# Performance work log

Hardware: AMD Instinct MI355X
Metric: run time of the kernel (lower is better)

The kernel has to match this reference:

```python
import jax, jax.numpy as jnp
import numpy as np

SEQ, B, IN_DIM, HID, DEPTH = 200, 128, 1024, 1024, 5
P_IN, P_HID = 0.75, 0.25  # input_dropout, hidden_dropout


def setup_inputs() -> dict:
    key = jax.random.key(0)
    ks = jax.random.split(key, 12)
    inp = jax.random.normal(ks[0], (SEQ, B, IN_DIM), dtype=jnp.float32)
    hidden = jax.random.normal(ks[1], (B, HID), dtype=jnp.float32) * 0.1

    # make_dropout_mask: bernoulli(keep_p) / keep_p ; tied_noise=True -> shared H/T masks
    keep_in, keep_hid = 1.0 - P_IN, 1.0 - P_HID
    h_mask = jax.random.bernoulli(ks[2], keep_in, (B, IN_DIM)).astype(jnp.float32) / keep_in
    s_mask = jax.random.bernoulli(ks[3], keep_hid, (B, HID)).astype(jnp.float32) / keep_hid

    # nn.Linear default init: U(-1/sqrt(fan_in), 1/sqrt(fan_in)); W stored (out, in)
    si, sh = 1.0 / np.sqrt(IN_DIM), 1.0 / np.sqrt(HID)
    u = lambda k, shape, s: jax.random.uniform(k, shape, jnp.float32, -s, s)
    Wih = u(ks[4], (HID, IN_DIM), si)
    bih = u(ks[5], (HID,), si)
    Wit = u(ks[6], (HID, IN_DIM), si)
    bit = u(ks[7], (HID,), si)
    Wh = u(ks[8], (DEPTH, HID, HID), sh)
    Wt = u(ks[9], (DEPTH, HID, HID), sh)
    # layer 0 recurrent Linears have bias=False -> zero bias row
    bh = u(ks[10], (DEPTH, HID), sh).at[0].set(0.0)
    bt = u(ks[11], (DEPTH, HID), sh).at[0].set(0.0)

    return {"inp": inp, "hidden": hidden, "h_mask": h_mask, "s_mask": s_mask,
            "Wih": Wih, "bih": bih, "Wit": Wit, "bit": bit,
            "Wh": Wh, "bh": bh, "Wt": Wt, "bt": bt}


def reference(inp, hidden, h_mask, s_mask, Wih, bih, Wit, bit, Wh, bh, Wt, bt):
    # tied_noise=True: same input mask for H and T paths, same hidden mask for both gates
    x = inp * h_mask  # (S, B, in) broadcast mask over seq
    H = jnp.einsum('sbi,oi->sbo', x, Wih) + bih  # precomputed input contribution
    T = jnp.einsum('sbi,oi->sbo', x, Wit) + bit

    def step(s, HT):
        H_t, T_t = HT  # (B, HID) each
        for l in range(DEPTH):
            sm = s * s_mask  # hidden dropout mask, shared H/T (tied_noise)
            if l == 0:
                Hl = jnp.tanh(H_t + jnp.einsum('bi,oi->bo', sm, Wh[l]) + bh[l])
                Tl = jax.nn.sigmoid(T_t + jnp.einsum('bi,oi->bo', sm, Wt[l]) + bt[l])
            else:
                Hl = jnp.tanh(jnp.einsum('bi,oi->bo', sm, Wh[l]) + bh[l])
                Tl = jax.nn.sigmoid(jnp.einsum('bi,oi->bo', sm, Wt[l]) + bt[l])
            # coupled highway: s_l = (h - s_{l-1}) * t + s_{l-1}
            s = (Hl - s) * Tl + s
        return s, s

    last, outs = jax.lax.scan(step, hidden, (H, T))
    return outs, last
```

## Files before the change

### kernel.cpp

```cpp
#include <hip/hip_runtime.h>
#include <hip/hip_bf16.h>
#include <stdint.h>

#define SEQ    200
#define BATCH  128
#define NHID   1024
#define NDEPTH 5
#define NBLK   256
#define GRP_BLK 128
#define CPB    8
#define PANEL  ((size_t)BATCH * NHID)
#define SB     (SEQ * BATCH)

typedef __bf16 bf16x8 __attribute__((ext_vector_type(8)));
typedef float  f32x4  __attribute__((ext_vector_type(4)));
typedef uint32_t u32x4 __attribute__((ext_vector_type(4)));
typedef __hip_bfloat16 bf16_t;

__device__ __forceinline__ f32x4 mfma16(bf16x8 a, bf16x8 b, f32x4 c) {
    return __builtin_amdgcn_mfma_f32_16x16x32_bf16(a, b, c, 0, 0, 0);
}
__device__ __forceinline__ bf16x8 as_bf16x8(u32x4 x) {
    union { u32x4 u; bf16x8 b; } t; t.u = x; return t.b;
}
__device__ __forceinline__ unsigned short f32_to_bf16_bits(float f) {
    uint32_t x = __float_as_uint(f);
    uint32_t r = ((x >> 16) & 1u) + 0x7fffu;
    return (unsigned short)((x + r) >> 16);
}
template<int PAT>
__device__ __forceinline__ float swzf(float v) {
    return __int_as_float(__builtin_amdgcn_ds_swizzle(__float_as_int(v), PAT));
}
template<int PAT>
__device__ __forceinline__ uint32_t swzu(uint32_t v) {
    return (uint32_t)__builtin_amdgcn_ds_swizzle((int)v, PAT);
}

__global__ void k_cast_bf16(const float* __restrict__ src, bf16_t* __restrict__ dst, int n) {
    for (int i = blockIdx.x * blockDim.x + threadIdx.x; i < n; i += gridDim.x * blockDim.x)
        dst[i] = __float2bfloat16(src[i]);
}

__global__ void k_init_smb(const float* __restrict__ hidden, const float* __restrict__ s_mask,
                           bf16_t* __restrict__ smb, int n) {
    for (int i = blockIdx.x * blockDim.x + threadIdx.x; i < n; i += gridDim.x * blockDim.x)
        smb[i] = __float2bfloat16(hidden[i] * s_mask[i]);
}

__global__ __launch_bounds__(256) void k_ht(
    const float* __restrict__ inp, const float* __restrict__ h_mask,
    const bf16_t* __restrict__ Wihb, const float* __restrict__ bih,
    const bf16_t* __restrict__ Witb, const float* __restrict__ bitv,
    _Float16* __restrict__ ht)
{
    const int lane = threadIdx.x & 63;
    const int w    = threadIdx.x >> 6;
    const int r0   = blockIdx.y * 32 + (w >> 1) * 16;
    const int c0   = blockIdx.x * 64 + (w & 1) * 32;
    const int lr   = lane & 15;
    const int kg   = lane >> 4;

    f32x4 aH0 = {0,0,0,0}, aH1 = {0,0,0,0}, aT0 = {0,0,0,0}, aT1 = {0,0,0,0};
    const int R = r0 + lr;
    const float* ap = inp + (size_t)R * NHID + kg * 8;
    const float* mp = h_mask + (size_t)(R & 127) * NHID + kg * 8;
    const bf16_t* Bh = Wihb + (size_t)(c0 + lr) * NHID + kg * 8;
    const bf16_t* Bt = Witb + (size_t)(c0 + lr) * NHID + kg * 8;

    for (int k = 0; k < NHID; k += 32) {
        f32x4 x0 = *(const f32x4*)(ap + k), x1 = *(const f32x4*)(ap + k + 4);
        f32x4 m0 = *(const f32x4*)(mp + k), m1 = *(const f32x4*)(mp + k + 4);
        union { bf16_t h[8]; bf16x8 v; } af;
        #pragma unroll
        for (int q = 0; q < 4; ++q) {
            af.h[q]     = __float2bfloat16(x0[q] * m0[q]);
            af.h[q + 4] = __float2bfloat16(x1[q] * m1[q]);
        }
        bf16x8 bh0 = *(const bf16x8*)(Bh + k);
        bf16x8 bh1 = *(const bf16x8*)(Bh + (size_t)16 * NHID + k);
        bf16x8 bt0 = *(const bf16x8*)(Bt + k);
        bf16x8 bt1 = *(const bf16x8*)(Bt + (size_t)16 * NHID + k);
        aH0 = mfma16(af.v, bh0, aH0);
        aH1 = mfma16(af.v, bh1, aH1);
        aT0 = mfma16(af.v, bt0, aT0);
        aT1 = mfma16(af.v, bt1, aT1);
    }

    const int n0 = c0 + lr, n1 = n0 + 16;
    #pragma unroll
    for (int j = 0; j < 4; ++j) {
        const int R2 = r0 + kg * 4 + j;
        const int t = R2 >> 7, b = R2 & 127;
        _Float16* hrow = ht + ((size_t)(t * 2 + 0) * BATCH + b) * NHID;
        _Float16* trow = ht + ((size_t)(t * 2 + 1) * BATCH + b) * NHID;
        hrow[n0] = (_Float16)(aH0[j] + bih[n0]);
        hrow[n1] = (_Float16)(aH1[j] + bih[n1]);
        trow[n0] = (_Float16)(aT0[j] + bitv[n0]);
        trow[n1] = (_Float16)(aT1[j] + bitv[n1]);
    }
}

#define LDU(i, OFF)  asm volatile("global_load_dwordx4 %0, %1, off offset:" OFF " sc0 sc1" \
                                  : "=v"(AR[i]) : "v"(aptr));
#define ISSUE32(M) \
    M(0,"0")    M(1,"64")   M(2,"128")  M(3,"192")  M(4,"256")  M(5,"320")  M(6,"384")  M(7,"448") \
    M(8,"512")  M(9,"576")  M(10,"640") M(11,"704") M(12,"768") M(13,"832") M(14,"896") M(15,"960") \
    M(16,"1024") M(17,"1088") M(18,"1152") M(19,"1216") M(20,"1280") M(21,"1344") M(22,"1408") M(23,"1472") \
    M(24,"1536") M(25,"1600") M(26,"1664") M(27,"1728") M(28,"1792") M(29,"1856") M(30,"1920") M(31,"1984")
#define WAITV(N) do { asm volatile("s_waitcnt vmcnt(" #N ")" ::: "memory"); \
                      __builtin_amdgcn_sched_barrier(0x187); } while (0)
#define CHUNK_LDS(c) do { _Pragma("unroll") \
    for (int e = 0; e < 8; ++e) { \
        const int off = (kg * 16 + ((c) * 8 + e) * 64) ^ xmask; \
        bf16x8 bf = *(const bf16x8*)(rowb + off); \
        acc = mfma16(as_bf16x8(AR[(c) * 8 + e]), bf, acc); } } while (0)

__global__ __launch_bounds__(256, 1) void k_rhn_persist(
    const float* __restrict__ hidden, const float* __restrict__ s_mask,
    const float* __restrict__ Wh,  const float* __restrict__ bh,
    const float* __restrict__ Wt,  const float* __restrict__ bt,
    const _Float16* __restrict__ ht,
    bf16_t* __restrict__ smbA, bf16_t* __restrict__ smbB,
    unsigned int* __restrict__ flags,
    float* __restrict__ out)
{
    extern __shared__ char wlds[];
    const int tid  = threadIdx.x;
    const int lane = tid & 63;
    const int wv   = tid >> 6;
    const int g    = blockIdx.x >> 7;
    const int gb   = blockIdx.x & (GRP_BLK - 1);
    const int c0   = gb * CPB;
    const int lr   = lane & 15;
    const int kg   = lane >> 4;
    const int wbase = g * 64 + wv * 16;
    const int cc   = c0 + (lr & 7);
    const bool isT = lr >= 8;
    const int xmask = (lr & 7) << 4;

    for (int row = wv; row < 80; row += 4) {
        const int l = row >> 4, r = row & 15;
        const float* src = ((r < 8) ? Wh : Wt) + ((size_t)l * NHID + c0 + (r & 7)) * NHID;
        char* rb = wlds + (size_t)row * 2048;
        const int X = (r & 7) << 4;
        #pragma unroll
        for (int u = 0; u < 2; ++u) {
            union { bf16_t h[8]; u32x4 v; } pk;
            #pragma unroll
            for (int q = 0; q < 8; ++q)
                pk.h[q] = __float2bfloat16(src[lane * 16 + u * 8 + q]);
            *(u32x4*)(rb + ((lane * 32 + u * 16) ^ X)) = pk.v;
        }
    }

    float biasl[NDEPTH];
    #pragma unroll
    for (int l = 0; l < NDEPTH; ++l)
        biasl[l] = isT ? bt[(size_t)l * NHID + cc] : bh[(size_t)l * NHID + cc];
    float sreg[4], smk[4];
    #pragma unroll
    for (int j = 0; j < 4; ++j) {
        const int row = wbase + kg * 4 + j;
        sreg[j] = hidden[(size_t)row * NHID + cc];
        smk[j]  = s_mask[(size_t)row * NHID + cc];
    }

    __syncthreads();

    const size_t aoff = (size_t)(wbase + lr) * NHID + kg * 8;
    unsigned int rv = 0;
    int par = 0;

    for (int t = 0; t < SEQ; ++t) {
        #pragma unroll
        for (int l = 0; l < NDEPTH; ++l) {
            const bf16_t* Abuf = par ? smbB : smbA;
            bf16_t*       An   = par ? smbA : smbB;
            f32x4 acc = {0.f, 0.f, 0.f, 0.f};
            u32x4 AR[32];

            {
                const bf16_t* aptr = Abuf + aoff;
                const char* rowb = wlds + (size_t)(l * 16 + lr) * 2048;
                ISSUE32(LDU)
                WAITV(24); CHUNK_LDS(0);
                WAITV(16); CHUNK_LDS(1);
                WAITV(8);  CHUNK_LDS(2);
                WAITV(0);  CHUNK_LDS(3);
            }
            if (l == 0) {
                const _Float16* hp = ht + (size_t)(t * 2 + (isT ? 1 : 0)) * PANEL + cc;
                #pragma unroll
                for (int j = 0; j < 4; ++j)
                    acc[j] += (float)hp[(size_t)(wbase + kg * 4 + j) * NHID];
            }

            const float vb = biasl[l];
            #pragma unroll
            for (int j = 0; j < 4; ++j) {
                float v = acc[j] + vb;
                float o = swzf<0x201F>(v);
                float Hv = tanhf(v);
                float Tv = 1.f / (1.f + __expf(-o));
                float sv = sreg[j];
                float sn = (Hv - sv) * Tv + sv;
                sreg[j] = sn;
                const int row = wbase + kg * 4 + j;

                uint32_t a  = (uint32_t)f32_to_bf16_bits(sn * smk[j]);
                uint32_t b1 = swzu<0x041F>(a);
                uint32_t w  = (a & 0xffffu) | (b1 << 16);
                uint32_t c2 = swzu<0x081F>(w);
                uint32_t e1 = swzu<0x101F>(w);
                uint32_t e2 = swzu<0x101F>(c2);
                if (lr == 0) {
                    uint64_t q0 = (uint64_t)w  | ((uint64_t)c2 << 32);
                    uint64_t q1 = (uint64_t)e1 | ((uint64_t)e2 << 32);
                    uint64_t* p = (uint64_t*)(An + (size_t)row * NHID + c0);
                    __hip_atomic_store(p,     q0, __ATOMIC_RELAXED, __HIP_MEMORY_SCOPE_AGENT);
                    __hip_atomic_store(p + 1, q1, __ATOMIC_RELAXED, __HIP_MEMORY_SCOPE_AGENT);
                }
                if (l == NDEPTH - 1 && lr < 8) {
                    out[((size_t)t * BATCH + row) * NHID + cc] = sn;
                    if (t == SEQ - 1)
                        out[(size_t)SEQ * BATCH * NHID + (size_t)row * NHID + cc] = sn;
                }
            }

            ++rv;
            if (!(t == SEQ - 1 && l == NDEPTH - 1)) {
                __syncthreads();
                if (tid == 0)
                    __hip_atomic_store(&flags[(g * GRP_BLK + gb) * 16], rv,
                                       __ATOMIC_RELAXED, __HIP_MEMORY_SCOPE_AGENT);
                if (tid < 64) {
                    const unsigned int* p0 = &flags[(g * GRP_BLK + lane) * 16];
                    const unsigned int* p1 = &flags[(g * GRP_BLK + 64 + lane) * 16];
                    for (;;) {
                        unsigned int f0 = __hip_atomic_load(p0, __ATOMIC_RELAXED,
                                                            __HIP_MEMORY_SCOPE_AGENT);
                        unsigned int f1 = __hip_atomic_load(p1, __ATOMIC_RELAXED,
                                                            __HIP_MEMORY_SCOPE_AGENT);
                        if (__all(f0 >= rv && f1 >= rv)) break;
                        __builtin_amdgcn_s_sleep(2);
                    }
                }
                __syncthreads();
            }
            par ^= 1;
        }
    }
}

extern "C" void kernel_launch(void* const* d_in, const int* in_sizes, int n_in,
                              void* d_out, int out_size, void* d_ws, size_t ws_size,
                              hipStream_t stream) {
    (void)in_sizes; (void)n_in; (void)out_size; (void)ws_size;

    const float* inp    = (const float*)d_in[0];
    const float* hidden = (const float*)d_in[1];
    const float* h_mask = (const float*)d_in[2];
    const float* s_mask = (const float*)d_in[3];
    const float* Wih    = (const float*)d_in[4];
    const float* bih    = (const float*)d_in[5];
    const float* Wit    = (const float*)d_in[6];
    const float* bitv   = (const float*)d_in[7];
    const float* Wh     = (const float*)d_in[8];
    const float* bh     = (const float*)d_in[9];
    const float* Wt     = (const float*)d_in[10];
    const float* bt     = (const float*)d_in[11];
    float* out = (float*)d_out;

    _Float16* ht   = (_Float16*)d_ws;
    bf16_t* Wihb   = (bf16_t*)(ht + (size_t)SEQ * 2 * PANEL);
    bf16_t* Witb   = Wihb + (size_t)NHID * NHID;
    bf16_t* smbA   = Witb + (size_t)NHID * NHID;
    bf16_t* smbB   = smbA + PANEL;
    unsigned int* flags = (unsigned int*)(smbB + PANEL);

    hipMemsetAsync(flags, 0, NBLK * 16 * sizeof(unsigned int), stream);
    k_cast_bf16<<<dim3(512), dim3(256), 0, stream>>>(Wih, Wihb, NHID * NHID);
    k_cast_bf16<<<dim3(512), dim3(256), 0, stream>>>(Wit, Witb, NHID * NHID);
    k_init_smb<<<dim3(64), dim3(256), 0, stream>>>(hidden, s_mask, smbA, BATCH * NHID);
    k_ht<<<dim3(NHID / 64, SB / 32), dim3(256), 0, stream>>>(
        inp, h_mask, Wihb, bih, Witb, bitv, ht);

    const size_t ldsBytes = (size_t)80 * 2048;
    hipFuncSetAttribute((const void*)k_rhn_persist,
                        hipFuncAttributeMaxDynamicSharedMemorySize, (int)ldsBytes);
    k_rhn_persist<<<dim3(NBLK), dim3(256), ldsBytes, stream>>>(
        hidden, s_mask, Wh, bh, Wt, bt, ht, smbA, smbB, flags, out);
}
```

Baseline: 7.644 ms.

## Relay hidden-state panel into per-XCD mirror buffers with two-level barrier

Each layer step now copies the freshly written bf16 hidden panel from the global buffer into a per-XCD mirror, split across the blocks on that XCD. The GEMM A-loads then read the mirror with sc0 only, so they can hit the XCD-local L2 instead of bypassing it. The grid-wide barrier now waits on all 256 blocks rather than two groups of 128, and an extra per-XCD barrier follows the relay. This trades cross-die uncached reads for an extra copy pass and a second synchronization every layer step. The mirrors reuse the Wih/Wit bf16 workspace, which is free after k_ht finishes.

```diff
diff --git a/kernel.cpp b/kernel.cpp
--- a/kernel.cpp
+++ b/kernel.cpp
@@ -10,6 +10,7 @@
 #define GRP_BLK 128
 #define CPB    8
 #define PANEL  ((size_t)BATCH * NHID)
+#define PANELB ((size_t)BATCH * NHID * 2)
 #define SB     (SEQ * BATCH)
 
 typedef __bf16 bf16x8 __attribute__((ext_vector_type(8)));
@@ -35,6 +36,11 @@
 template<int PAT>
 __device__ __forceinline__ uint32_t swzu(uint32_t v) {
     return (uint32_t)__builtin_amdgcn_ds_swizzle((int)v, PAT);
+}
+__device__ __forceinline__ int get_xcc_id() {
+    int x;
+    asm volatile("s_getreg_b32 %0, hwreg(HW_REG_XCC_ID)" : "=s"(x));
+    return x & 7;
 }
 
 __global__ void k_cast_bf16(const float* __restrict__ src, bf16_t* __restrict__ dst, int n) {
@@ -101,8 +107,8 @@
     }
 }
 
-#define LDU(i, OFF)  asm volatile("global_load_dwordx4 %0, %1, off offset:" OFF " sc0 sc1" \
-                                  : "=v"(AR[i]) : "v"(aptr));
+#define LDU(i, OFF) asm volatile("global_load_dwordx4 %0, %1, off offset:" OFF " sc0" \
+                                 : "=v"(AR[i]) : "v"(aptr));
 #define ISSUE32(M) \
     M(0,"0")    M(1,"64")   M(2,"128")  M(3,"192")  M(4,"256")  M(5,"320")  M(6,"384")  M(7,"448") \
     M(8,"512")  M(9,"576")  M(10,"640") M(11,"704") M(12,"768") M(13,"832") M(14,"896") M(15,"960") \
@@ -112,9 +118,20 @@
                       __builtin_amdgcn_sched_barrier(0x187); } while (0)
 #define CHUNK_LDS(c) do { _Pragma("unroll") \
     for (int e = 0; e < 8; ++e) { \
-        const int off = (kg * 16 + ((c) * 8 + e) * 64) ^ xmask; \
-        bf16x8 bf = *(const bf16x8*)(rowb + off); \
+        bf16x8 bf = *(const bf16x8*)(rowb + ((kg * 16 + ((c) * 8 + e) * 64) ^ xmask)); \
         acc = mfma16(as_bf16x8(AR[(c) * 8 + e]), bf, acc); } } while (0)
+
+__device__ __forceinline__ void relay(const char* __restrict__ src, char* __restrict__ dst,
+                                      size_t b0, size_t b1, int tid, int nthr) {
+    for (size_t o = b0 + (size_t)tid * 32; o < b1; o += (size_t)nthr * 32) {
+        u32x4 v0, v1;
+        asm volatile("global_load_dwordx4 %0, %1, off sc0 sc1" : "=v"(v0) : "v"(src + o));
+        asm volatile("global_load_dwordx4 %0, %1, off sc0 sc1" : "=v"(v1) : "v"(src + o + 16));
+        asm volatile("s_waitcnt vmcnt(0)" ::: "memory");
+        *(u32x4*)(dst + o) = v0;
+        *(u32x4*)(dst + o + 16) = v1;
+    }
+}
 
 __global__ __launch_bounds__(256, 1) void k_rhn_persist(
     const float* __restrict__ hidden, const float* __restrict__ s_mask,
@@ -122,7 +139,11 @@
     const float* __restrict__ Wt,  const float* __restrict__ bt,
     const _Float16* __restrict__ ht,
     bf16_t* __restrict__ smbA, bf16_t* __restrict__ smbB,
+    bf16_t* __restrict__ mir,
     unsigned int* __restrict__ flags,
+    unsigned int* __restrict__ xcdcnt,
+    unsigned int* __restrict__ lflags,
+    unsigned int* __restrict__ ranks,
     float* __restrict__ out)
 {
     extern __shared__ char wlds[];
@@ -138,6 +159,14 @@
     const int cc   = c0 + (lr & 7);
     const bool isT = lr >= 8;
     const int xmask = (lr & 7) << 4;
+    const int xcd  = get_xcc_id();
+
+    if (tid == 0) {
+        unsigned int r = __hip_atomic_fetch_add(&xcdcnt[xcd * 16], 1u,
+                                                __ATOMIC_RELAXED, __HIP_MEMORY_SCOPE_AGENT);
+        __hip_atomic_store(&ranks[blockIdx.x * 16], r,
+                           __ATOMIC_RELAXED, __HIP_MEMORY_SCOPE_AGENT);
+    }
 
     for (int row = wv; row < 80; row += 4) {
         const int l = row >> 4, r = row & 15;
@@ -168,20 +197,61 @@
 
     __syncthreads();
 
+    unsigned int rv = 1;
+    {
+        if (tid == 0)
+            __hip_atomic_store(&flags[blockIdx.x * 16], rv,
+                               __ATOMIC_RELAXED, __HIP_MEMORY_SCOPE_AGENT);
+        if (tid < 64) {
+            const unsigned int* p0 = &flags[lane * 16];
+            const unsigned int* p1 = &flags[(64 + lane) * 16];
+            const unsigned int* p2 = &flags[(128 + lane) * 16];
+            const unsigned int* p3 = &flags[(192 + lane) * 16];
+            for (;;) {
+                unsigned int f0 = __hip_atomic_load(p0, __ATOMIC_RELAXED, __HIP_MEMORY_SCOPE_AGENT);
+                unsigned int f1 = __hip_atomic_load(p1, __ATOMIC_RELAXED, __HIP_MEMORY_SCOPE_AGENT);
+                unsigned int f2 = __hip_atomic_load(p2, __ATOMIC_RELAXED, __HIP_MEMORY_SCOPE_AGENT);
+                unsigned int f3 = __hip_atomic_load(p3, __ATOMIC_RELAXED, __HIP_MEMORY_SCOPE_AGENT);
+                if (__all(f0 >= rv && f1 >= rv && f2 >= rv && f3 >= rv)) break;
+                __builtin_amdgcn_s_sleep(2);
+            }
+        }
+        __syncthreads();
+    }
+
+    const int lrank = (int)__hip_atomic_load(&ranks[blockIdx.x * 16],
+                                             __ATOMIC_RELAXED, __HIP_MEMORY_SCOPE_AGENT);
+    const int cnt   = (int)__hip_atomic_load(&xcdcnt[xcd * 16],
+                                             __ATOMIC_RELAXED, __HIP_MEMORY_SCOPE_AGENT);
+    const size_t chunks = PANELB / 32;
+    const size_t b0 = ((size_t)lrank * chunks / cnt) * 32;
+    const size_t b1 = ((size_t)(lrank + 1) * chunks / cnt) * 32;
+
+    bf16_t* mirx = mir + (size_t)xcd * 2 * PANEL;
+    relay((const char*)smbA, (char*)mirx, b0, b1, tid, 256);
+    __syncthreads();
+    if (tid == 0)
+        __hip_atomic_store(&lflags[(xcd * 64 + lrank) * 16], rv,
+                           __ATOMIC_RELAXED, __HIP_MEMORY_SCOPE_AGENT);
+    if (tid < 64)
+        for (int s = lane; s < cnt; s += 64)
+            while (__hip_atomic_load(&lflags[(xcd * 64 + s) * 16],
+                                     __ATOMIC_RELAXED, __HIP_MEMORY_SCOPE_AGENT) < rv)
+                __builtin_amdgcn_s_sleep(1);
+    __syncthreads();
+
     const size_t aoff = (size_t)(wbase + lr) * NHID + kg * 8;
-    unsigned int rv = 0;
     int par = 0;
 
     for (int t = 0; t < SEQ; ++t) {
         #pragma unroll
         for (int l = 0; l < NDEPTH; ++l) {
-            const bf16_t* Abuf = par ? smbB : smbA;
-            bf16_t*       An   = par ? smbA : smbB;
+            bf16_t* An = par ? smbA : smbB;
             f32x4 acc = {0.f, 0.f, 0.f, 0.f};
             u32x4 AR[32];
 
             {
-                const bf16_t* aptr = Abuf + aoff;
+                const bf16_t* aptr = mirx + (size_t)par * PANEL + aoff;
                 const char* rowb = wlds + (size_t)(l * 16 + lr) * 2048;
                 ISSUE32(LDU)
                 WAITV(24); CHUNK_LDS(0);
@@ -209,8 +279,8 @@
                 const int row = wbase + kg * 4 + j;
 
                 uint32_t a  = (uint32_t)f32_to_bf16_bits(sn * smk[j]);
-                uint32_t b1 = swzu<0x041F>(a);
-                uint32_t w  = (a & 0xffffu) | (b1 << 16);
+                uint32_t b1w = swzu<0x041F>(a);
+                uint32_t w  = (a & 0xffffu) | (b1w << 16);
                 uint32_t c2 = swzu<0x081F>(w);
                 uint32_t e1 = swzu<0x101F>(w);
                 uint32_t e2 = swzu<0x101F>(c2);
@@ -232,20 +302,35 @@
             if (!(t == SEQ - 1 && l == NDEPTH - 1)) {
                 __syncthreads();
                 if (tid == 0)
-                    __hip_atomic_store(&flags[(g * GRP_BLK + gb) * 16], rv,
+                    __hip_atomic_store(&flags[blockIdx.x * 16], rv,
                                        __ATOMIC_RELAXED, __HIP_MEMORY_SCOPE_AGENT);
                 if (tid < 64) {
-                    const unsigned int* p0 = &flags[(g * GRP_BLK + lane) * 16];
-                    const unsigned int* p1 = &flags[(g * GRP_BLK + 64 + lane) * 16];
+                    const unsigned int* p0 = &flags[lane * 16];
+                    const unsigned int* p1 = &flags[(64 + lane) * 16];
+                    const unsigned int* p2 = &flags[(128 + lane) * 16];
+                    const unsigned int* p3 = &flags[(192 + lane) * 16];
                     for (;;) {
-                        unsigned int f0 = __hip_atomic_load(p0, __ATOMIC_RELAXED,
-                                                            __HIP_MEMORY_SCOPE_AGENT);
-                        unsigned int f1 = __hip_atomic_load(p1, __ATOMIC_RELAXED,
-                                                            __HIP_MEMORY_SCOPE_AGENT);
-                        if (__all(f0 >= rv && f1 >= rv)) break;
+                        unsigned int f0 = __hip_atomic_load(p0, __ATOMIC_RELAXED, __HIP_MEMORY_SCOPE_AGENT);
+                        unsigned int f1 = __hip_atomic_load(p1, __ATOMIC_RELAXED, __HIP_MEMORY_SCOPE_AGENT);
+                        unsigned int f2 = __hip_atomic_load(p2, __ATOMIC_RELAXED, __HIP_MEMORY_SCOPE_AGENT);
+                        unsigned int f3 = __hip_atomic_load(p3, __ATOMIC_RELAXED, __HIP_MEMORY_SCOPE_AGENT);
+                        if (__all(f0 >= rv && f1 >= rv && f2 >= rv && f3 >= rv)) break;
                         __builtin_amdgcn_s_sleep(2);
                     }
                 }
+                __syncthreads();
+
+                relay((const char*)An, (char*)(mirx + (size_t)(par ^ 1) * PANEL),
+                      b0, b1, tid, 256);
+                __syncthreads();
+                if (tid == 0)
+                    __hip_atomic_store(&lflags[(xcd * 64 + lrank) * 16], rv,
+                                       __ATOMIC_RELAXED, __HIP_MEMORY_SCOPE_AGENT);
+                if (tid < 64)
+                    for (int s = lane; s < cnt; s += 64)
+                        while (__hip_atomic_load(&lflags[(xcd * 64 + s) * 16],
+                                                 __ATOMIC_RELAXED, __HIP_MEMORY_SCOPE_AGENT) < rv)
+                            __builtin_amdgcn_s_sleep(1);
                 __syncthreads();
             }
             par ^= 1;
@@ -275,11 +360,16 @@
     _Float16* ht   = (_Float16*)d_ws;
     bf16_t* Wihb   = (bf16_t*)(ht + (size_t)SEQ * 2 * PANEL);
     bf16_t* Witb   = Wihb + (size_t)NHID * NHID;
+    bf16_t* mir    = Wihb;
     bf16_t* smbA   = Witb + (size_t)NHID * NHID;
     bf16_t* smbB   = smbA + PANEL;
-    unsigned int* flags = (unsigned int*)(smbB + PANEL);
-
-    hipMemsetAsync(flags, 0, NBLK * 16 * sizeof(unsigned int), stream);
+    unsigned int* flags  = (unsigned int*)(smbB + PANEL);
+    unsigned int* xcdcnt = flags  + NBLK * 16;
+    unsigned int* lflags = xcdcnt + 8 * 16;
+    unsigned int* ranks  = lflags + 8 * 64 * 16;
+    const size_t ctl_u32 = (size_t)(NBLK * 16 + 8 * 16 + 8 * 64 * 16 + NBLK * 16);
+
+    hipMemsetAsync(flags, 0, ctl_u32 * sizeof(unsigned int), stream);
     k_cast_bf16<<<dim3(512), dim3(256), 0, stream>>>(Wih, Wihb, NHID * NHID);
     k_cast_bf16<<<dim3(512), dim3(256), 0, stream>>>(Wit, Witb, NHID * NHID);
     k_init_smb<<<dim3(64), dim3(256), 0, stream>>>(hidden, s_mask, smbA, BATCH * NHID);
@@ -290,5 +380,6 @@
     hipFuncSetAttribute((const void*)k_rhn_persist,
                         hipFuncAttributeMaxDynamicSharedMemorySize, (int)ldsBytes);
     k_rhn_persist<<<dim3(NBLK), dim3(256), ldsBytes, stream>>>(
-        hidden, s_mask, Wh, bh, Wt, bt, ht, smbA, smbB, flags, out);
-}
+        hidden, s_mask, Wh, bh, Wt, bt, ht, smbA, smbB, mir,
+        flags, xcdcnt, lflags, ranks, out);
+}
```

After: 9.664 ms. +26.4%, slower.
